# Optimization experiments

Hardware: AMD Instinct MI355X
Metric: run time of the kernel (lower is better)

The kernel has to match this reference:

```python
import jax, jax.numpy as jnp
import numpy as np

H, W = 56, 56
N = H * W
C = 2
THETA_ALPHA = 160.0
THETA_BETA = 3.0
THETA_GAMMA = 3.0
NUM_ITERATIONS = 10


def setup_inputs() -> dict:
    key = jax.random.key(0)
    k1, k2, k3, k4 = jax.random.split(key, 4)
    inputs = jax.random.uniform(k1, (2, H, W), dtype=jnp.float32)
    # Keras 'uniform' initializer: U(-0.05, 0.05)
    sp_w = jax.random.uniform(k2, (C, C), minval=-0.05, maxval=0.05, dtype=jnp.float32)
    bl_w = jax.random.uniform(k3, (C, C), minval=-0.05, maxval=0.05, dtype=jnp.float32)
    compat = jax.random.uniform(k4, (C, C), minval=-0.05, maxval=0.05, dtype=jnp.float32)
    return {"inputs": inputs, "spatial_ker_weights": sp_w,
            "bilateral_ker_weights": bl_w, "compatibility_matrix": compat}


def _sqdist(f):
    # f: [N, D] -> [N, N] squared pairwise distances
    s = jnp.sum(f * f, axis=1)
    return s[:, None] + s[None, :] - 2.0 * (f @ f.T)


def _kernels(rgb_flat):
    # rgb_flat: [N, 3] pixel colors (0..255)
    ys, xs = jnp.meshgrid(jnp.arange(H, dtype=jnp.float32),
                          jnp.arange(W, dtype=jnp.float32), indexing="ij")
    pos = jnp.stack([xs.reshape(-1), ys.reshape(-1)], axis=1)  # [N, 2]
    # spatial (Gaussian) kernel: exp(-||p-q||^2 / (2*gamma^2))
    k_sp = jnp.exp(-0.5 * _sqdist(pos / THETA_GAMMA))
    # bilateral kernel: positions scaled by alpha, colors by beta
    f_bl = jnp.concatenate([pos / THETA_ALPHA, rgb_flat / THETA_BETA], axis=1)
    k_bl = jnp.exp(-0.5 * _sqdist(f_bl))
    return k_sp, k_bl


def reference(inputs, spatial_ker_weights, bilateral_ker_weights, compatibility_matrix):
    unary = inputs[0]            # [H, W], foreground prob
    gray = inputs[1] * 255.0     # [H, W], image intensities scaled as in the layer

    # unaries: [C, H, W] with channel 0 = 1-u, channel 1 = u
    unaries = jnp.stack([1.0 - unary, unary], axis=0).reshape(C, N)

    rgb_flat = jnp.tile(gray.reshape(-1)[:, None], (1, 3))  # [N, 3]

    k_sp, k_bl = _kernels(rgb_flat)
    ones = jnp.ones((N,), dtype=jnp.float32)
    norm_sp = k_sp @ ones  # [N]
    norm_bl = k_bl @ ones  # [N]

    q = unaries
    for i in range(NUM_ITERATIONS):
        softmax_out = q if i == 0 else jax.nn.softmax(q, axis=0)
        spatial_out = (softmax_out @ k_sp) / norm_sp[None, :]     # [C, N]
        bilateral_out = (softmax_out @ k_bl) / norm_bl[None, :]   # [C, N]
        message = spatial_ker_weights @ spatial_out + bilateral_ker_weights @ bilateral_out
        pairwise = compatibility_matrix @ message                 # [C, N]
        q = unaries - pairwise

    cur_q = q.reshape(C, H, W).transpose(1, 2, 0)  # [H, W, C]
    obj_prob = jax.nn.softmax(cur_q, axis=2)[:, :, 1]
    return obj_prob.reshape(1, H, W)
```

## Files before the change

kernel.cpp:

```cpp
#include <hip/hip_runtime.h>


namespace {

constexpr int NPIX = 3136;
constexpr int WIMG = 56;
constexpr int JPB  = 16;
constexpr int NBLK = NPIX / JPB;
constexpr int NTHR = 512;
constexpr int NQ   = NPIX / 4;
constexpr int NBUF = 9;
constexpr int Q2   = NQ - NTHR;
constexpr int NBIN = 128;
constexpr int BANDB = 9;
constexpr int NCHK = 98;
constexpr int CPX  = 32;

constexpr float LOG2E = 1.4426950408889634f;
constexpr float C1 = -LOG2E / 18.0f;
constexpr float C2 = -LOG2E / 51200.0f;
constexpr float C3 = -LOG2E / 6.0f;

constexpr int O_SSH  = 0;
constexpr int O_SSRT = 12544;
constexpr int O_GXY  = 25088;
constexpr int O_MSRT = 50176;
constexpr int O_RANK = 56448;
constexpr int O_OFF  = 62720;
constexpr int O_WSX  = 63248;
constexpr int O_WSY  = 66832;
constexpr int O_LIDX = 70416;
constexpr int POOLSZ = 73552;

#define REDUCE32(v) \
    { v += __shfl_xor(v, 1); v += __shfl_xor(v, 2); v += __shfl_xor(v, 4); \
      v += __shfl_xor(v, 8); v += __shfl_xor(v, 16); }
#define REDUCE64(v) \
    { v += __shfl_xor(v, 1); v += __shfl_xor(v, 2); v += __shfl_xor(v, 4); \
      v += __shfl_xor(v, 8); v += __shfl_xor(v, 16); v += __shfl_xor(v, 32); }

__global__ __launch_bounds__(NTHR) void crf_all(
    const float* __restrict__ inp,
    const float* __restrict__ spw, const float* __restrict__ blw,
    const float* __restrict__ cmw,
    float* sbufs, float* __restrict__ out)
{
    __shared__ __align__(16) unsigned char pool[POOLSZ];
    float*  s_sh  = (float*)(pool + O_SSH);
    float4* s_sh4 = (float4*)(pool + O_SSH);
    float*  s_srt = (float*)(pool + O_SSRT);
    float2* gxy   = (float2*)(pool + O_GXY);
    unsigned short* m_srt = (unsigned short*)(pool + O_MSRT);
    unsigned short* rank  = (unsigned short*)(pool + O_RANK);
    unsigned*       offs  = (unsigned*)(pool + O_OFF);
    float*  wsx   = (float*)(pool + O_WSX);
    float*  wsy   = (float*)(pool + O_WSY);
    unsigned char*  lidx = (unsigned char*)(pool + O_LIDX);
    unsigned short* H  = (unsigned short*)(pool + O_SSH);
    unsigned*       Hz = (unsigned*)(pool + O_SSH);

    const int t   = threadIdx.x;
    const int bid = blockIdx.x;
    const int sub = t & 31;
    const int jl  = t >> 5;
    const int j   = bid * JPB + jl;
    const int xj  = j % WIMG;
    const int yj  = j / WIMG;
    const float xjf = (float)xj, yjf = (float)yj;

    const float uj = inp[j];
    const float gj = inp[NPIX + j] * 255.0f;

    const float e0 = cmw[2] - cmw[0];
    const float e1 = cmw[3] - cmw[1];
    const float alpha = e0 * (spw[0] + blw[0]) + e1 * (spw[2] + blw[2]);
    const float beta  = e0 * (spw[1] - spw[0]) + e1 * (spw[3] - spw[2]);
    const float gamma = e0 * (blw[1] - blw[0]) + e1 * (blw[3] - blw[2]);

    for (int i = t; i < 6272; i += NTHR) Hz[i] = 0u;
    for (int idx = t; idx < JPB * 56; idx += NTHR) {
        const int jlw = idx / 56, p = idx - jlw * 56;
        const int jj = bid * JPB + jlw;
        const float ddx = (float)(jj % WIMG - p);
        const float ddy = (float)(jj / WIMG - p);
        wsx[idx] = __builtin_amdgcn_exp2f(C1 * ddx * ddx);
        wsy[idx] = __builtin_amdgcn_exp2f(C1 * ddy * ddy);
    }
    __syncthreads();
    if (t < NCHK) {
        unsigned short* Hr = H + t * NBIN;
        const int mb = t * CPX;
        for (int i = 0; i < CPX; ++i) {
            int b = (int)(inp[NPIX + mb + i] * 255.0f);
            b = (b > 255 ? 255 : b) >> 1;
            lidx[mb + i] = (unsigned char)Hr[b];
            Hr[b] = (unsigned short)(Hr[b] + 1);
        }
    }
    __syncthreads();
    if (t < NBIN) {
        unsigned run = 0;
        for (int c = 0; c < NCHK; ++c) {
            unsigned short v = H[c * NBIN + t];
            H[c * NBIN + t] = (unsigned short)run;
            run += v;
        }
        offs[t] = run;
    }
    __syncthreads();
    if (t < 64) {
        unsigned v0 = offs[2 * t], v1 = offs[2 * t + 1];
        unsigned sum = v0 + v1;
        unsigned sc = sum;
        for (int d = 1; d < 64; d <<= 1) {
            unsigned n = __shfl_up(sc, d);
            if (t >= d) sc += n;
        }
        unsigned base = sc - sum;
        offs[2 * t] = base;
        offs[2 * t + 1] = base + v0;
        if (t == 63) offs[NBIN] = sc;
    }
    __syncthreads();
    for (int m = t; m < NPIX; m += NTHR) {
        int b = (int)(inp[NPIX + m] * 255.0f);
        b = (b > 255 ? 255 : b) >> 1;
        const int r = (int)offs[b] + (int)H[(m >> 5) * NBIN + b] + (int)lidx[m];
        m_srt[r] = (unsigned short)m;
        rank[m]  = (unsigned short)r;
    }
    __syncthreads();
    for (int p = t; p < NPIX; p += NTHR) {
        const int m = (int)m_srt[p];
        s_srt[p] = inp[m];
        const int yi = (m * 9363) >> 19;
        const int xi = m - yi * 56;
        gxy[p] = make_float2(inp[NPIX + m] * 255.0f, (float)(xi + 64 * yi));
    }
    {
        const float4* u4 = (const float4*)inp;
        for (int q = t; q < NQ; q += NTHR) s_sh4[q] = u4[q];
    }
    __syncthreads();

    float sx, sy;
    {
        float dd = xjf - (float)sub;
        sx = __builtin_amdgcn_exp2f(C1 * dd * dd);
        if (sub + 32 < 56) {
            float d2 = xjf - (float)(sub + 32);
            sx += __builtin_amdgcn_exp2f(C1 * d2 * d2);
        }
        REDUCE32(sx);
        dd = yjf - (float)sub;
        sy = __builtin_amdgcn_exp2f(C1 * dd * dd);
        if (sub + 32 < 56) {
            float d2 = yjf - (float)(sub + 32);
            sy += __builtin_amdgcn_exp2f(C1 * d2 * d2);
        }
        REDUCE32(sy);
    }
    const float rnsp = 1.0f / (sx * sy);

    int bj = (int)gj; bj = (bj > 255 ? 255 : bj) >> 1;
    const int b0 = bj < BANDB ? 0 : bj - BANDB;
    const int b1 = bj + BANDB > NBIN - 1 ? NBIN - 1 : bj + BANDB;
    const int blo = (int)offs[b0];
    const int bhi = (int)offs[b1 + 1];

    auto spatial = [&]() -> float {
        const int wv = t >> 6;
        const int ln = t & 63;
        float v0 = 0.f, v1 = 0.f;
        if (ln < 56) {
            const float4* S = s_sh4 + ln * 14;
            float4 sv[14];
#pragma unroll
            for (int q = 0; q < 14; ++q) sv[q] = S[q];
            const int c0 = wv * 2, c1 = c0 + 1;
            const float4* R0 = (const float4*)(wsx + c0 * 56);
            const float4* R1 = (const float4*)(wsx + c1 * 56);
            float a0 = 0.f, a1 = 0.f;
#pragma unroll
            for (int q = 0; q < 14; ++q) {
                float4 w0 = R0[q], w1 = R1[q];
                a0 = fmaf(w0.x, sv[q].x, a0); a0 = fmaf(w0.y, sv[q].y, a0);
                a0 = fmaf(w0.z, sv[q].z, a0); a0 = fmaf(w0.w, sv[q].w, a0);
                a1 = fmaf(w1.x, sv[q].x, a1); a1 = fmaf(w1.y, sv[q].y, a1);
                a1 = fmaf(w1.z, sv[q].z, a1); a1 = fmaf(w1.w, sv[q].w, a1);
            }
            v0 = wsy[c0 * 56 + ln] * a0;
            v1 = wsy[c1 * 56 + ln] * a1;
        }
        REDUCE64(v0); REDUCE64(v1);
        return (ln < 32) ? v0 : v1;
    };

    auto bilateral = [&](float* nacc_out) -> float {
        float acc = 0.f, nacc = 0.f;
#pragma unroll 2
        for (int p = blo + sub; p < bhi; p += 32) {
            const float2 gx = gxy[p];
            const float sv  = s_srt[p];
            const float yi  = floorf(gx.y * 0.015625f);
            const float xi  = fmaf(-64.f, yi, gx.y);
            const float ux = xi - xjf, vy = yi - yjf;
            const float r2 = fmaf(ux, ux, vy * vy);
            const float dg = gx.x - gj;
            const float w = __builtin_amdgcn_exp2f(fmaf(dg * C3, dg, r2 * C2));
            acc = fmaf(w, sv, acc);
            if (nacc_out) nacc += w;
        }
        REDUCE32(acc);
        if (nacc_out) { REDUCE32(nacc); *nacc_out = nacc; }
        return acc;
    };

    auto publish_sync = [&](float s, float* buf) {
        if (sub == 0)
            __hip_atomic_store(&buf[j], s, __ATOMIC_RELAXED,
                               __HIP_MEMORY_SCOPE_AGENT);
        const float4* src = (const float4*)buf;
        float4 a, b;
        const bool two = (t < Q2);
        bool da = false, db = !two;
        for (;;) {
            if (!da)
                asm volatile("global_load_dwordx4 %0, %1, off sc0 sc1"
                             : "=&v"(a) : "v"(src + t));
            if (!db)
                asm volatile("global_load_dwordx4 %0, %1, off sc0 sc1"
                             : "=&v"(b) : "v"(src + NTHR + t));
            asm volatile("s_waitcnt vmcnt(0)" ::: "memory");
            if (!da) da = (fminf(fminf(a.x, a.y), fminf(a.z, a.w)) != 0.0f);
            if (!db) db = (fminf(fminf(b.x, b.y), fminf(b.z, b.w)) != 0.0f);
            if (da && db) break;
        }
        s_sh4[t] = a;
        {
            const int p4 = 4 * t;
            s_srt[rank[p4 + 0]] = a.x;
            s_srt[rank[p4 + 1]] = a.y;
            s_srt[rank[p4 + 2]] = a.z;
            s_srt[rank[p4 + 3]] = a.w;
        }
        if (two) {
            s_sh4[NTHR + t] = b;
            const int p4 = 4 * (NTHR + t);
            s_srt[rank[p4 + 0]] = b.x;
            s_srt[rank[p4 + 1]] = b.y;
            s_srt[rank[p4 + 2]] = b.z;
            s_srt[rank[p4 + 3]] = b.w;
        }
        __syncthreads();
    };

    const float base = 2.0f * uj - 1.0f - alpha;
    float rnbl, s;

    {
        float tsp = spatial();
        float nacc;
        float acc = bilateral(&nacc);
        rnbl = 1.0f / nacc;
        float d = base - beta * (tsp * rnsp) - gamma * (acc * rnbl);
        s = 1.0f / (1.0f + __builtin_amdgcn_exp2f(-d * LOG2E));
    }
    publish_sync(s, sbufs);

    for (int k = 1; k < 10; ++k) {
        float tsp = spatial();
        float acc = bilateral(nullptr);
        float d = base - beta * (tsp * rnsp) - gamma * (acc * rnbl);
        s = 1.0f / (1.0f + __builtin_amdgcn_exp2f(-d * LOG2E));
        if (k < 9) publish_sync(s, sbufs + k * NPIX);
        else if (sub == 0) out[j] = s;
    }
}

}

extern "C" void kernel_launch(void* const* d_in, const int* in_sizes, int n_in,
                              void* d_out, int out_size, void* d_ws, size_t ws_size,
                              hipStream_t stream) {
    const float* inp = (const float*)d_in[0];
    const float* spw = (const float*)d_in[1];
    const float* blw = (const float*)d_in[2];
    const float* cmw = (const float*)d_in[3];
    float* sbufs = (float*)d_ws;
    float* out = (float*)d_out;

    hipMemsetAsync(sbufs, 0, NBUF * NPIX * sizeof(float), stream);
    crf_all<<<dim3(NBLK), dim3(NTHR), 0, stream>>>(inp, spw, blw, cmw,
                                                   sbufs, out);
}
```

Measured before the change: 62.16 us.

## Assign one full wavefront per pixel with 1024-thread blocks

Doubles the block size so each output pixel is handled by a full 64-lane wavefront instead of half a wavefront. The bilateral band loop strides by 64, the spatial matvec uses one row per wave, and the polling publish loop gives each thread a single float4 instead of two. This shortens each wave's serial loop and lets the spin loop issue one load per thread. In exchange the block carries more threads and registers, which may reduce how many blocks fit per CU in the cooperative grid and adds more polling threads.

```diff
diff --git a/kernel.cpp b/kernel.cpp
--- a/kernel.cpp
+++ b/kernel.cpp
@@ -7,10 +7,9 @@
 constexpr int WIMG = 56;
 constexpr int JPB  = 16;
 constexpr int NBLK = NPIX / JPB;
-constexpr int NTHR = 512;
+constexpr int NTHR = 1024;
 constexpr int NQ   = NPIX / 4;
 constexpr int NBUF = 9;
-constexpr int Q2   = NQ - NTHR;
 constexpr int NBIN = 128;
 constexpr int BANDB = 9;
 constexpr int NCHK = 98;
@@ -32,9 +31,6 @@
 constexpr int O_LIDX = 70416;
 constexpr int POOLSZ = 73552;
 
-#define REDUCE32(v) \
-    { v += __shfl_xor(v, 1); v += __shfl_xor(v, 2); v += __shfl_xor(v, 4); \
-      v += __shfl_xor(v, 8); v += __shfl_xor(v, 16); }
 #define REDUCE64(v) \
     { v += __shfl_xor(v, 1); v += __shfl_xor(v, 2); v += __shfl_xor(v, 4); \
       v += __shfl_xor(v, 8); v += __shfl_xor(v, 16); v += __shfl_xor(v, 32); }
@@ -61,8 +57,8 @@
 
     const int t   = threadIdx.x;
     const int bid = blockIdx.x;
-    const int sub = t & 31;
-    const int jl  = t >> 5;
+    const int sub = t & 63;
+    const int jl  = t >> 6;
     const int j   = bid * JPB + jl;
     const int xj  = j % WIMG;
     const int yj  = j / WIMG;
@@ -143,23 +139,14 @@
     }
     __syncthreads();
 
-    float sx, sy;
-    {
+    float sx = 0.f, sy = 0.f;
+    if (sub < 56) {
         float dd = xjf - (float)sub;
         sx = __builtin_amdgcn_exp2f(C1 * dd * dd);
-        if (sub + 32 < 56) {
-            float d2 = xjf - (float)(sub + 32);
-            sx += __builtin_amdgcn_exp2f(C1 * d2 * d2);
-        }
-        REDUCE32(sx);
         dd = yjf - (float)sub;
         sy = __builtin_amdgcn_exp2f(C1 * dd * dd);
-        if (sub + 32 < 56) {
-            float d2 = yjf - (float)(sub + 32);
-            sy += __builtin_amdgcn_exp2f(C1 * d2 * d2);
-        }
-        REDUCE32(sy);
-    }
+    }
+    REDUCE64(sx); REDUCE64(sy);
     const float rnsp = 1.0f / (sx * sy);
 
     int bj = (int)gj; bj = (bj > 255 ? 255 : bj) >> 1;
@@ -169,37 +156,30 @@
     const int bhi = (int)offs[b1 + 1];
 
     auto spatial = [&]() -> float {
-        const int wv = t >> 6;
-        const int ln = t & 63;
-        float v0 = 0.f, v1 = 0.f;
-        if (ln < 56) {
-            const float4* S = s_sh4 + ln * 14;
+        float v0 = 0.f;
+        if (sub < 56) {
+            const float4* S = s_sh4 + sub * 14;
             float4 sv[14];
 #pragma unroll
             for (int q = 0; q < 14; ++q) sv[q] = S[q];
-            const int c0 = wv * 2, c1 = c0 + 1;
-            const float4* R0 = (const float4*)(wsx + c0 * 56);
-            const float4* R1 = (const float4*)(wsx + c1 * 56);
-            float a0 = 0.f, a1 = 0.f;
+            const float4* R = (const float4*)(wsx + jl * 56);
+            float a0 = 0.f;
 #pragma unroll
             for (int q = 0; q < 14; ++q) {
-                float4 w0 = R0[q], w1 = R1[q];
-                a0 = fmaf(w0.x, sv[q].x, a0); a0 = fmaf(w0.y, sv[q].y, a0);
-                a0 = fmaf(w0.z, sv[q].z, a0); a0 = fmaf(w0.w, sv[q].w, a0);
-                a1 = fmaf(w1.x, sv[q].x, a1); a1 = fmaf(w1.y, sv[q].y, a1);
-                a1 = fmaf(w1.z, sv[q].z, a1); a1 = fmaf(w1.w, sv[q].w, a1);
+                float4 w = R[q];
+                a0 = fmaf(w.x, sv[q].x, a0); a0 = fmaf(w.y, sv[q].y, a0);
+                a0 = fmaf(w.z, sv[q].z, a0); a0 = fmaf(w.w, sv[q].w, a0);
             }
-            v0 = wsy[c0 * 56 + ln] * a0;
-            v1 = wsy[c1 * 56 + ln] * a1;
-        }
-        REDUCE64(v0); REDUCE64(v1);
-        return (ln < 32) ? v0 : v1;
+            v0 = wsy[jl * 56 + sub] * a0;
+        }
+        REDUCE64(v0);
+        return v0;
     };
 
     auto bilateral = [&](float* nacc_out) -> float {
         float acc = 0.f, nacc = 0.f;
 #pragma unroll 2
-        for (int p = blo + sub; p < bhi; p += 32) {
+        for (int p = blo + sub; p < bhi; p += 64) {
             const float2 gx = gxy[p];
             const float sv  = s_srt[p];
             const float yi  = floorf(gx.y * 0.015625f);
@@ -211,8 +191,8 @@
             acc = fmaf(w, sv, acc);
             if (nacc_out) nacc += w;
         }
-        REDUCE32(acc);
-        if (nacc_out) { REDUCE32(nacc); *nacc_out = nacc; }
+        REDUCE64(acc);
+        if (nacc_out) { REDUCE64(nacc); *nacc_out = nacc; }
         return acc;
     };
 
@@ -220,37 +200,21 @@
         if (sub == 0)
             __hip_atomic_store(&buf[j], s, __ATOMIC_RELAXED,
                                __HIP_MEMORY_SCOPE_AGENT);
-        const float4* src = (const float4*)buf;
-        float4 a, b;
-        const bool two = (t < Q2);
-        bool da = false, db = !two;
-        for (;;) {
-            if (!da)
+        if (t < NQ) {
+            const float4* src = (const float4*)buf;
+            float4 a;
+            for (;;) {
                 asm volatile("global_load_dwordx4 %0, %1, off sc0 sc1"
                              : "=&v"(a) : "v"(src + t));
-            if (!db)
-                asm volatile("global_load_dwordx4 %0, %1, off sc0 sc1"
-                             : "=&v"(b) : "v"(src + NTHR + t));
-            asm volatile("s_waitcnt vmcnt(0)" ::: "memory");
-            if (!da) da = (fminf(fminf(a.x, a.y), fminf(a.z, a.w)) != 0.0f);
-            if (!db) db = (fminf(fminf(b.x, b.y), fminf(b.z, b.w)) != 0.0f);
-            if (da && db) break;
-        }
-        s_sh4[t] = a;
-        {
+                asm volatile("s_waitcnt vmcnt(0)" ::: "memory");
+                if (fminf(fminf(a.x, a.y), fminf(a.z, a.w)) != 0.0f) break;
+            }
+            s_sh4[t] = a;
             const int p4 = 4 * t;
             s_srt[rank[p4 + 0]] = a.x;
             s_srt[rank[p4 + 1]] = a.y;
             s_srt[rank[p4 + 2]] = a.z;
             s_srt[rank[p4 + 3]] = a.w;
-        }
-        if (two) {
-            s_sh4[NTHR + t] = b;
-            const int p4 = 4 * (NTHR + t);
-            s_srt[rank[p4 + 0]] = b.x;
-            s_srt[rank[p4 + 1]] = b.y;
-            s_srt[rank[p4 + 2]] = b.z;
-            s_srt[rank[p4 + 3]] = b.w;
         }
         __syncthreads();
     };
```

New measurement: 92.51 us. 1.49x slower.
